# Kernel tuning notes

Measured on AMD Instinct MI355X. Metric: run time of the kernel, lower is better.

The kernel has to match this reference:

```python
import jax, jax.numpy as jnp
import numpy as np

S = 1048576   # sequence length (only free scale knob)
D = 20        # d_model (forced == d_internal by the original code)
DI = 20       # d_internal (forced to 20 by output_i[:20])
C = 3         # num_classes
L = 2         # num_layers


def setup_inputs() -> dict:
    key = jax.random.key(0)
    ks = jax.random.split(key, 13)
    f = lambda k, shp, s=1.0: jax.random.normal(k, shp, dtype=jnp.float32) * s
    return {
        "indices": f(ks[0], (S, D)),
        # per-layer stacked parameters (leading axis L)
        "Wq":   f(ks[1], (L, DI, D)),          # torch.randn(d_internal, d)
        "Wk":   f(ks[2], (L, DI, D)),
        "Wv":   f(ks[3], (L, D, D)),           # torch.randn(d, d)
        "Wres": f(ks[4], (L, D, DI)),          # W_residual: (d, d_internal)
        "W1":   f(ks[5], (L, D, DI), 0.2),     # Linear(d_internal, d_model).weight
        "b1":   f(ks[6], (L, D), 0.2),
        "W2":   f(ks[7], (L, D, DI), 0.2),     # second Linear(d_internal, d_model)
        "b2":   f(ks[8], (L, D), 0.2),
        "W3":   f(ks[9], (L, D, D), 0.2),      # Linear(input_dim=d, d_model) residual proj
        "b3":   f(ks[10], (L, D), 0.2),
        "Wc":   f(ks[11], (C, D), 0.2),        # final Linear(d_model, num_classes)
        "bc":   f(ks[12], (C,), 0.2),
    }


def _layer(x, Wq, Wk, Wv, Wres, W1, b1, W2, b2, W3, b3):
    # Vectorized form of the original per-token Python loop.
    q = x @ Wq.T                                   # (S, DI)
    k = x @ Wk.T                                   # (S, DI)
    v = x @ Wv.T                                   # (S, D)
    # scalar similarity per token; softmax over a singleton axis == 1.0 (kept for fidelity)
    sim = jnp.sum(q * k, axis=-1, keepdims=True) / np.sqrt(DI)   # (S, 1)
    p = jax.nn.softmax(sim, axis=-1)               # all ones
    out = (p * v)[:, :DI]                          # output_i = v_i[:20]
    out = out + x @ Wres                           # residual via W_residual
    out = jax.nn.relu(out @ W1.T + b1)             # linear1 + relu
    out = out @ W2.T + b2                          # linear2
    out = out + x @ W3.T + b3                      # final input residual projection
    return out


def reference(indices, Wq, Wk, Wv, Wres, W1, b1, W2, b2, W3, b3, Wc, bc):
    x = indices
    for l in range(L):  # small fixed layer count
        x = _layer(x, Wq[l], Wk[l], Wv[l], Wres[l], W1[l], b1[l], W2[l], b2[l], W3[l], b3[l])
    logits = x @ Wc.T + bc                         # (S, C)
    return jax.nn.softmax(logits, axis=1)
```

## Files before the change

### kernel.cpp

```cpp
#include <hip/hip_runtime.h>
#include <math.h>


#define OFF_G1   0
#define OFF_P1   400
#define OFF_P2   800
#define OFF_M2T  1200
#define OFF_Q1T  1280
#define OFF_Q2T  1360
#define OFF_B11  1440
#define OFF_F2   1460
#define OFF_F3   1480
#define NWTOT    1484

__global__ void prep_kernel(const float* __restrict__ Wv, const float* __restrict__ Wres,
                            const float* __restrict__ W1, const float* __restrict__ b1,
                            const float* __restrict__ W2, const float* __restrict__ b2,
                            const float* __restrict__ W3, const float* __restrict__ b3,
                            const float* __restrict__ Wc, const float* __restrict__ bc,
                            float* __restrict__ W) {
    __shared__ float G2[400];
    __shared__ float M3[60];
    __shared__ float e1[20];
    const int tid = threadIdx.x;
    for (int idx = tid; idx < 480; idx += 256) {
        if (idx < 400) {
            const int i = idx / 20, m = idx % 20;
            float s = 0.f;
            for (int j = 0; j < 20; ++j)
                s = fmaf(Wv[400 + j*20 + i] + Wres[400 + i*20 + j], W1[400 + m*20 + j], s);
            G2[idx] = s;
        } else if (idx < 460) {
            const int r = idx - 400, i = r / 3, c = r % 3;
            float s = 0.f;
            for (int p = 0; p < 20; ++p)
                s = fmaf(Wc[c*20 + p], W3[400 + p*20 + i], s);
            M3[r] = s;
        } else {
            const int j = idx - 460;
            e1[j] = b2[j] + b3[j];
        }
    }
    __syncthreads();
    for (int idx = tid; idx < NWTOT; idx += 256) {
        float s = 0.f;
        if (idx < 400) {
            const int k = idx / 20, m = idx % 20;
            for (int j = 0; j < 20; ++j)
                s = fmaf(Wv[j*20 + k] + Wres[k*20 + j], W1[m*20 + j], s);
        } else if (idx < 800) {
            const int r = idx - 400, mp = r / 20, m = r % 20;
            for (int i = 0; i < 20; ++i)
                s = fmaf(W2[i*20 + mp], G2[i*20 + m], s);
        } else if (idx < 1200) {
            const int r = idx - 800, k = r / 20, m = r % 20;
            for (int i = 0; i < 20; ++i)
                s = fmaf(W3[i*20 + k], G2[i*20 + m], s);
        } else if (idx < 1280) {
            const int r = idx - 1200, m = r / 4, c = r % 4;
            if (c < 3)
                for (int p = 0; p < 20; ++p)
                    s = fmaf(Wc[c*20 + p], W2[400 + p*20 + m], s);
        } else if (idx < 1360) {
            const int r = idx - 1280, k = r / 4, c = r % 4;
            if (c < 3)
                for (int i = 0; i < 20; ++i)
                    s = fmaf(W2[i*20 + k], M3[i*3 + c], s);
        } else if (idx < 1440) {
            const int r = idx - 1360, k = r / 4, c = r % 4;
            if (c < 3)
                for (int i = 0; i < 20; ++i)
                    s = fmaf(W3[i*20 + k], M3[i*3 + c], s);
        } else if (idx < 1460) {
            s = b1[idx - 1440];
        } else if (idx < 1480) {
            const int m = idx - 1460;
            s = b1[20 + m];
            for (int i = 0; i < 20; ++i)
                s = fmaf(e1[i], G2[i*20 + m], s);
        } else {
            const int c = idx - 1480;
            if (c < 3) {
                s = bc[c];
                for (int p = 0; p < 20; ++p)
                    s = fmaf(Wc[c*20 + p], b2[20 + p] + b3[20 + p], s);
                for (int i = 0; i < 20; ++i)
                    s = fmaf(e1[i], M3[i*3 + c], s);
            }
        }
        W[idx] = s;
    }
}

typedef float v4f __attribute__((ext_vector_type(4)));
typedef const __attribute__((address_space(4))) v4f  c4f_t;
typedef const __attribute__((address_space(4))) float cfl_t;

__global__ __launch_bounds__(256, 6) void fwd_kernel(const float* __restrict__ X,
                                                     const float* __restrict__ Wg,
                                                     float* __restrict__ out, int ntok) {
    c4f_t* W4 = (c4f_t*)(unsigned long long)Wg;
    cfl_t* Wf = (cfl_t*)(unsigned long long)Wg;

    const int tid = blockIdx.x * blockDim.x + threadIdx.x;
    if (tid >= ntok) return;
    const float4* xp = reinterpret_cast<const float4*>(X + (size_t)tid * 20);

    float h[20], g[20], la[3];

    #pragma unroll
    for (int q = 0; q < 5; ++q) {
        const v4f b = W4[OFF_B11/4 + q];
        const v4f f = W4[OFF_F2/4 + q];
        h[4*q+0] = b.x; h[4*q+1] = b.y; h[4*q+2] = b.z; h[4*q+3] = b.w;
        g[4*q+0] = f.x; g[4*q+1] = f.y; g[4*q+2] = f.z; g[4*q+3] = f.w;
    }
    la[0] = Wf[OFF_F3 + 0]; la[1] = Wf[OFF_F3 + 1]; la[2] = Wf[OFF_F3 + 2];

    #pragma unroll
    for (int q = 0; q < 5; ++q) {
        const float4 xv = xp[q];
        float xc[4];
        xc[0] = xv.x; xc[1] = xv.y; xc[2] = xv.z; xc[3] = xv.w;
        #pragma unroll
        for (int d = 0; d < 4; ++d) {
            const int k = 4*q + d;
            const float xk = xc[d];
            const v4f wq2 = W4[OFF_Q2T/4 + k];
            la[0] = fmaf(xk, wq2.x, la[0]);
            la[1] = fmaf(xk, wq2.y, la[1]);
            la[2] = fmaf(xk, wq2.z, la[2]);
            #pragma unroll
            for (int r = 0; r < 5; ++r) {
                const v4f wg = W4[OFF_G1/4 + k*5 + r];
                h[4*r+0] = fmaf(xk, wg.x, h[4*r+0]);
                h[4*r+1] = fmaf(xk, wg.y, h[4*r+1]);
                h[4*r+2] = fmaf(xk, wg.z, h[4*r+2]);
                h[4*r+3] = fmaf(xk, wg.w, h[4*r+3]);
            }
            #pragma unroll
            for (int r = 0; r < 5; ++r) {
                const v4f wp = W4[OFF_P2/4 + k*5 + r];
                g[4*r+0] = fmaf(xk, wp.x, g[4*r+0]);
                g[4*r+1] = fmaf(xk, wp.y, g[4*r+1]);
                g[4*r+2] = fmaf(xk, wp.z, g[4*r+2]);
                g[4*r+3] = fmaf(xk, wp.w, g[4*r+3]);
            }
        }
    }

    #pragma unroll
    for (int i = 0; i < 20; ++i) h[i] = fmaxf(h[i], 0.f);

    #pragma unroll
    for (int k = 0; k < 20; ++k) {
        const float hk = h[k];
        const v4f wq1 = W4[OFF_Q1T/4 + k];
        la[0] = fmaf(hk, wq1.x, la[0]);
        la[1] = fmaf(hk, wq1.y, la[1]);
        la[2] = fmaf(hk, wq1.z, la[2]);
        #pragma unroll
        for (int r = 0; r < 5; ++r) {
            const v4f wp = W4[OFF_P1/4 + k*5 + r];
            g[4*r+0] = fmaf(hk, wp.x, g[4*r+0]);
            g[4*r+1] = fmaf(hk, wp.y, g[4*r+1]);
            g[4*r+2] = fmaf(hk, wp.z, g[4*r+2]);
            g[4*r+3] = fmaf(hk, wp.w, g[4*r+3]);
        }
    }

    #pragma unroll
    for (int i = 0; i < 20; ++i) g[i] = fmaxf(g[i], 0.f);

    #pragma unroll
    for (int k = 0; k < 20; ++k) {
        const float gk = g[k];
        const v4f wm = W4[OFF_M2T/4 + k];
        la[0] = fmaf(gk, wm.x, la[0]);
        la[1] = fmaf(gk, wm.y, la[1]);
        la[2] = fmaf(gk, wm.z, la[2]);
    }

    const float m = fmaxf(fmaxf(la[0], la[1]), la[2]);
    const float e0 = __expf(la[0] - m), e1 = __expf(la[1] - m), e2 = __expf(la[2] - m);
    const float r = 1.f / (e0 + e1 + e2);
    float* o = out + (size_t)tid * 3;
    o[0] = e0 * r;
    o[1] = e1 * r;
    o[2] = e2 * r;
}

extern "C" void kernel_launch(void* const* d_in, const int* in_sizes, int n_in,
                              void* d_out, int out_size, void* d_ws, size_t ws_size,
                              hipStream_t stream) {
    const float* X    = (const float*)d_in[0];
    const float* Wv   = (const float*)d_in[3];
    const float* Wres = (const float*)d_in[4];
    const float* W1   = (const float*)d_in[5];
    const float* b1   = (const float*)d_in[6];
    const float* W2   = (const float*)d_in[7];
    const float* b2   = (const float*)d_in[8];
    const float* W3   = (const float*)d_in[9];
    const float* b3   = (const float*)d_in[10];
    const float* Wc   = (const float*)d_in[11];
    const float* bc   = (const float*)d_in[12];
    float* out = (float*)d_out;
    float* W   = (float*)d_ws;

    const int S = in_sizes[0] / 20;

    prep_kernel<<<1, 256, 0, stream>>>(Wv, Wres, W1, b1, W2, b2, W3, b3, Wc, bc, W);

    const int block = 256;
    const int grid = (S + block - 1) / block;
    fwd_kernel<<<grid, block, 0, stream>>>(X, W, out, S);
}
```

Before: 172.5 us.

## Use packed FP32 FMAs with VGPR-addressed weight loads in forward kernel

Rewrites the per-token MLP chain to use two-wide vector FMAs (v_pk_fma_f32) on float2 accumulators, halving the FMA instruction count. The weights are now read through a pointer offset by an opaque VGPR zero, so the loads become per-lane vector memory loads instead of scalar constant loads. This frees the scalar path but adds vector-memory traffic. Launch bounds drop from 6 to 2 waves per SIMD, allowing more registers at the cost of occupancy.

```diff
diff --git a/kernel.cpp b/kernel.cpp
--- a/kernel.cpp
+++ b/kernel.cpp
@@ -92,30 +92,41 @@
     }
 }
 
+typedef float f2  __attribute__((ext_vector_type(2)));
 typedef float v4f __attribute__((ext_vector_type(4)));
-typedef const __attribute__((address_space(4))) v4f  c4f_t;
-typedef const __attribute__((address_space(4))) float cfl_t;
-
-__global__ __launch_bounds__(256, 6) void fwd_kernel(const float* __restrict__ X,
+
+__device__ __forceinline__ v4f ldw(const float* p) {
+    return *reinterpret_cast<const v4f*>(p);
+}
+
+__global__ __launch_bounds__(256, 2) void fwd_kernel(const float* __restrict__ X,
                                                      const float* __restrict__ Wg,
                                                      float* __restrict__ out, int ntok) {
-    c4f_t* W4 = (c4f_t*)(unsigned long long)Wg;
-    cfl_t* Wf = (cfl_t*)(unsigned long long)Wg;
+    int z;
+    asm volatile("v_mov_b32 %0, 0" : "=v"(z));
+    const float* Wd  = Wg + z;
+    const float* Wd2 = Wd + 800;
 
     const int tid = blockIdx.x * blockDim.x + threadIdx.x;
     if (tid >= ntok) return;
     const float4* xp = reinterpret_cast<const float4*>(X + (size_t)tid * 20);
 
-    float h[20], g[20], la[3];
+    f2 h2[10], g2[10], la2[2];
 
     #pragma unroll
     for (int q = 0; q < 5; ++q) {
-        const v4f b = W4[OFF_B11/4 + q];
-        const v4f f = W4[OFF_F2/4 + q];
-        h[4*q+0] = b.x; h[4*q+1] = b.y; h[4*q+2] = b.z; h[4*q+3] = b.w;
-        g[4*q+0] = f.x; g[4*q+1] = f.y; g[4*q+2] = f.z; g[4*q+3] = f.w;
-    }
-    la[0] = Wf[OFF_F3 + 0]; la[1] = Wf[OFF_F3 + 1]; la[2] = Wf[OFF_F3 + 2];
+        const v4f b = ldw(Wd2 + 640 + 4*q);
+        const v4f f = ldw(Wd2 + 660 + 4*q);
+        f2 blo = {b.x, b.y}, bhi = {b.z, b.w};
+        f2 flo = {f.x, f.y}, fhi = {f.z, f.w};
+        h2[2*q+0] = blo; h2[2*q+1] = bhi;
+        g2[2*q+0] = flo; g2[2*q+1] = fhi;
+    }
+    {
+        const v4f f3 = ldw(Wd2 + 680);
+        f2 lo = {f3.x, f3.y}, hi = {f3.z, f3.w};
+        la2[0] = lo; la2[1] = hi;
+    }
 
     #pragma unroll
     for (int q = 0; q < 5; ++q) {
@@ -126,63 +137,74 @@
         for (int d = 0; d < 4; ++d) {
             const int k = 4*q + d;
             const float xk = xc[d];
-            const v4f wq2 = W4[OFF_Q2T/4 + k];
-            la[0] = fmaf(xk, wq2.x, la[0]);
-            la[1] = fmaf(xk, wq2.y, la[1]);
-            la[2] = fmaf(xk, wq2.z, la[2]);
+            const f2 xkp = {xk, xk};
+            {
+                const v4f w = ldw(Wd2 + 560 + 4*k);
+                const f2 wlo = {w.x, w.y}, whi = {w.z, w.w};
+                la2[0] = __builtin_elementwise_fma(xkp, wlo, la2[0]);
+                la2[1] = __builtin_elementwise_fma(xkp, whi, la2[1]);
+            }
             #pragma unroll
             for (int r = 0; r < 5; ++r) {
-                const v4f wg = W4[OFF_G1/4 + k*5 + r];
-                h[4*r+0] = fmaf(xk, wg.x, h[4*r+0]);
-                h[4*r+1] = fmaf(xk, wg.y, h[4*r+1]);
-                h[4*r+2] = fmaf(xk, wg.z, h[4*r+2]);
-                h[4*r+3] = fmaf(xk, wg.w, h[4*r+3]);
+                const v4f w = ldw(Wd + k*20 + 4*r);
+                const f2 wlo = {w.x, w.y}, whi = {w.z, w.w};
+                h2[2*r+0] = __builtin_elementwise_fma(xkp, wlo, h2[2*r+0]);
+                h2[2*r+1] = __builtin_elementwise_fma(xkp, whi, h2[2*r+1]);
             }
             #pragma unroll
             for (int r = 0; r < 5; ++r) {
-                const v4f wp = W4[OFF_P2/4 + k*5 + r];
-                g[4*r+0] = fmaf(xk, wp.x, g[4*r+0]);
-                g[4*r+1] = fmaf(xk, wp.y, g[4*r+1]);
-                g[4*r+2] = fmaf(xk, wp.z, g[4*r+2]);
-                g[4*r+3] = fmaf(xk, wp.w, g[4*r+3]);
-            }
-        }
-    }
-
-    #pragma unroll
-    for (int i = 0; i < 20; ++i) h[i] = fmaxf(h[i], 0.f);
+                const v4f w = ldw(Wd2 + k*20 + 4*r);
+                const f2 wlo = {w.x, w.y}, whi = {w.z, w.w};
+                g2[2*r+0] = __builtin_elementwise_fma(xkp, wlo, g2[2*r+0]);
+                g2[2*r+1] = __builtin_elementwise_fma(xkp, whi, g2[2*r+1]);
+            }
+        }
+    }
+
+    {
+        const f2 z2 = {0.f, 0.f};
+        #pragma unroll
+        for (int p = 0; p < 10; ++p) h2[p] = __builtin_elementwise_max(h2[p], z2);
+    }
 
     #pragma unroll
     for (int k = 0; k < 20; ++k) {
-        const float hk = h[k];
-        const v4f wq1 = W4[OFF_Q1T/4 + k];
-        la[0] = fmaf(hk, wq1.x, la[0]);
-        la[1] = fmaf(hk, wq1.y, la[1]);
-        la[2] = fmaf(hk, wq1.z, la[2]);
+        const float hk = (k & 1) ? h2[k>>1].y : h2[k>>1].x;
+        const f2 hkp = {hk, hk};
+        {
+            const v4f w = ldw(Wd2 + 480 + 4*k);
+            const f2 wlo = {w.x, w.y}, whi = {w.z, w.w};
+            la2[0] = __builtin_elementwise_fma(hkp, wlo, la2[0]);
+            la2[1] = __builtin_elementwise_fma(hkp, whi, la2[1]);
+        }
         #pragma unroll
         for (int r = 0; r < 5; ++r) {
-            const v4f wp = W4[OFF_P1/4 + k*5 + r];
-            g[4*r+0] = fmaf(hk, wp.x, g[4*r+0]);
-            g[4*r+1] = fmaf(hk, wp.y, g[4*r+1]);
-            g[4*r+2] = fmaf(hk, wp.z, g[4*r+2]);
-            g[4*r+3] = fmaf(hk, wp.w, g[4*r+3]);
-        }
-    }
-
-    #pragma unroll
-    for (int i = 0; i < 20; ++i) g[i] = fmaxf(g[i], 0.f);
+            const v4f w = ldw(Wd + 400 + k*20 + 4*r);
+            const f2 wlo = {w.x, w.y}, whi = {w.z, w.w};
+            g2[2*r+0] = __builtin_elementwise_fma(hkp, wlo, g2[2*r+0]);
+            g2[2*r+1] = __builtin_elementwise_fma(hkp, whi, g2[2*r+1]);
+        }
+    }
+
+    {
+        const f2 z2 = {0.f, 0.f};
+        #pragma unroll
+        for (int p = 0; p < 10; ++p) g2[p] = __builtin_elementwise_max(g2[p], z2);
+    }
 
     #pragma unroll
     for (int k = 0; k < 20; ++k) {
-        const float gk = g[k];
-        const v4f wm = W4[OFF_M2T/4 + k];
-        la[0] = fmaf(gk, wm.x, la[0]);
-        la[1] = fmaf(gk, wm.y, la[1]);
-        la[2] = fmaf(gk, wm.z, la[2]);
-    }
-
-    const float m = fmaxf(fmaxf(la[0], la[1]), la[2]);
-    const float e0 = __expf(la[0] - m), e1 = __expf(la[1] - m), e2 = __expf(la[2] - m);
+        const float gk = (k & 1) ? g2[k>>1].y : g2[k>>1].x;
+        const f2 gkp = {gk, gk};
+        const v4f w = ldw(Wd2 + 400 + 4*k);
+        const f2 wlo = {w.x, w.y}, whi = {w.z, w.w};
+        la2[0] = __builtin_elementwise_fma(gkp, wlo, la2[0]);
+        la2[1] = __builtin_elementwise_fma(gkp, whi, la2[1]);
+    }
+
+    const float l0 = la2[0].x, l1 = la2[0].y, l2 = la2[1].x;
+    const float m = fmaxf(fmaxf(l0, l1), l2);
+    const float e0 = __expf(l0 - m), e1 = __expf(l1 - m), e2 = __expf(l2 - m);
     const float r = 1.f / (e0 + e1 + e2);
     float* o = out + (size_t)tid * 3;
     o[0] = e0 * r;
```

Measured after the change: 310.6 us. +80.0%, slower.
